# Performance work log

Measured on AMD Instinct MI355X. Metric: run time of the kernel, lower is better.

## Reference

```python
import jax, jax.numpy as jnp
import numpy as np

B, F = 4096, 16384          # batch, total features
G, S = 512, 32              # n_groups, group_size (F = G*S, contiguous partition)
UNITS = 1


def setup_inputs() -> dict:
    key = jax.random.key(0)
    k_x, k_w = jax.random.split(key)
    x = jax.random.normal(k_x, (B, F), dtype=jnp.float32)
    # contiguous non-overlapping groups: group g owns columns [g*S, (g+1)*S)
    group_idx = jnp.arange(G * S, dtype=jnp.int64).reshape(G, S)
    # per-group multiplicative-factor weights (GroupConnected.w, HeNormal ~ scaled normal)
    w_group = jax.random.normal(k_w, (G, S), dtype=jnp.float32) * jnp.sqrt(2.0 / S)
    # final Dense kernel, kernel_initializer=Ones in the original
    fc_kernel = jnp.ones((G, UNITS), dtype=jnp.float32)
    return {"x": x, "group_idx": group_idx, "w_group": w_group, "fc_kernel": fc_kernel}


def reference(x, group_idx, w_group, fc_kernel):
    # GroupConnected: per-group gather + weighted sum, vectorized as one gather + einsum.
    gathered = x[:, group_idx]                      # [B, G, S]
    gc = jnp.einsum('bgs,gs->bg', gathered, w_group)  # [B, G]
    # TibGroupLasso.fc: Dense(units, no bias)
    return gc @ fc_kernel                           # [B, units]
```

## Files before the change

kernel.cpp:

```cpp
#include <hip/hip_runtime.h>

#define BB 4096
#define FF 16384
#define GG 512
#define SS 32

typedef float v4f __attribute__((ext_vector_type(4)));

__global__ void build_v_kernel(const int* __restrict__ idx,
                               const float* __restrict__ w,
                               const float* __restrict__ fc,
                               float* __restrict__ v) {
    int i = blockIdx.x * blockDim.x + threadIdx.x;
    if (i < GG * SS) {
        v[idx[i]] = w[i] * fc[i >> 5];
    }
}

__global__ __launch_bounds__(256) void gemv_kernel(const float* __restrict__ x,
                                                   const float* __restrict__ v,
                                                   float* __restrict__ out) {
    const int wave = threadIdx.x >> 6;
    const int lane = threadIdx.x & 63;
    const int row  = (blockIdx.x << 2) + wave;

    const v4f* __restrict__ x4 = (const v4f*)(x + (size_t)row * FF);
    const v4f* __restrict__ v4 = (const v4f*)v;

    v4f acc0 = {0.0f, 0.0f, 0.0f, 0.0f};
    v4f acc1 = {0.0f, 0.0f, 0.0f, 0.0f};
    #pragma unroll 4
    for (int i = lane; i < FF / 4; i += 128) {
        v4f xa = __builtin_nontemporal_load(&x4[i]);
        v4f xb = __builtin_nontemporal_load(&x4[i + 64]);
        acc0 += xa * v4[i];
        acc1 += xb * v4[i + 64];
    }
    v4f acc = acc0 + acc1;
    float sum = (acc.x + acc.y) + (acc.z + acc.w);

    #pragma unroll
    for (int off = 32; off > 0; off >>= 1)
        sum += __shfl_down(sum, off, 64);

    if (lane == 0) out[row] = sum;
}

extern "C" void kernel_launch(void* const* d_in, const int* in_sizes, int n_in,
                              void* d_out, int out_size, void* d_ws, size_t ws_size,
                              hipStream_t stream) {
    const float* x   = (const float*)d_in[0];
    const int*   idx = (const int*)d_in[1];
    const float* w   = (const float*)d_in[2];
    const float* fc  = (const float*)d_in[3];
    float* out = (float*)d_out;
    float* v   = (float*)d_ws;

    build_v_kernel<<<(GG * SS + 255) / 256, 256, 0, stream>>>(idx, w, fc, v);
    gemv_kernel<<<BB / 4, 256, 0, stream>>>(x, v, out);
}
```

Measured before the change: 338.1 us.

## Split GEMV columns in halves, stage weight vector in LDS, add combine pass

Each block now handles four rows over one half of the feature dimension and first copies that half of the weight vector (32 KB) into shared memory. The kernel then reads the vector from LDS instead of global memory. Partial sums are written to workspace and a third kernel adds the two halves. This doubles the block count and cuts global traffic for the vector, at the cost of an extra launch, a per-block LDS fill with a barrier, and lower occupancy from the 32 KB of shared memory per block.

```diff
diff --git a/kernel.cpp b/kernel.cpp
--- a/kernel.cpp
+++ b/kernel.cpp
@@ -4,6 +4,7 @@
 #define FF 16384
 #define GG 512
 #define SS 32
+#define HALF (FF / 2)
 
 typedef float v4f __attribute__((ext_vector_type(4)));
 
@@ -17,24 +18,35 @@
     }
 }
 
-__global__ __launch_bounds__(256) void gemv_kernel(const float* __restrict__ x,
-                                                   const float* __restrict__ v,
-                                                   float* __restrict__ out) {
-    const int wave = threadIdx.x >> 6;
-    const int lane = threadIdx.x & 63;
-    const int row  = (blockIdx.x << 2) + wave;
+__global__ __launch_bounds__(256, 4) void gemv_kernel(const float* __restrict__ x,
+                                                      const float* __restrict__ v,
+                                                      float* __restrict__ part) {
+    __shared__ v4f vs[HALF / 4];
 
-    const v4f* __restrict__ x4 = (const v4f*)(x + (size_t)row * FF);
-    const v4f* __restrict__ v4 = (const v4f*)v;
+    const int c  = blockIdx.x & 1;
+    const int r0 = (blockIdx.x >> 1) << 2;
+    const int tid = threadIdx.x;
+
+    const v4f* __restrict__ vg = (const v4f*)(v + c * HALF);
+    #pragma unroll
+    for (int i = tid; i < HALF / 4; i += 256)
+        vs[i] = vg[i];
+    __syncthreads();
+
+    const int wave = tid >> 6;
+    const int lane = tid & 63;
+    const int row  = r0 + wave;
+
+    const v4f* __restrict__ x4 = (const v4f*)(x + (size_t)row * FF + c * HALF);
 
     v4f acc0 = {0.0f, 0.0f, 0.0f, 0.0f};
     v4f acc1 = {0.0f, 0.0f, 0.0f, 0.0f};
     #pragma unroll 4
-    for (int i = lane; i < FF / 4; i += 128) {
+    for (int i = lane; i < HALF / 4; i += 128) {
         v4f xa = __builtin_nontemporal_load(&x4[i]);
         v4f xb = __builtin_nontemporal_load(&x4[i + 64]);
-        acc0 += xa * v4[i];
-        acc1 += xb * v4[i + 64];
+        acc0 += xa * vs[i];
+        acc1 += xb * vs[i + 64];
     }
     v4f acc = acc0 + acc1;
     float sum = (acc.x + acc.y) + (acc.z + acc.w);
@@ -43,7 +55,13 @@
     for (int off = 32; off > 0; off >>= 1)
         sum += __shfl_down(sum, off, 64);
 
-    if (lane == 0) out[row] = sum;
+    if (lane == 0) part[c * BB + row] = sum;
+}
+
+__global__ void combine_kernel(const float* __restrict__ part,
+                               float* __restrict__ out) {
+    int i = blockIdx.x * blockDim.x + threadIdx.x;
+    if (i < BB) out[i] = part[i] + part[BB + i];
 }
 
 extern "C" void kernel_launch(void* const* d_in, const int* in_sizes, int n_in,
@@ -54,8 +72,10 @@
     const float* w   = (const float*)d_in[2];
     const float* fc  = (const float*)d_in[3];
     float* out = (float*)d_out;
-    float* v   = (float*)d_ws;
+    float* v    = (float*)d_ws;
+    float* part = v + FF;
 
     build_v_kernel<<<(GG * SS + 255) / 256, 256, 0, stream>>>(idx, w, fc, v);
-    gemv_kernel<<<BB / 4, 256, 0, stream>>>(x, v, out);
+    gemv_kernel<<<2 * (BB / 4), 256, 0, stream>>>(x, v, part);
+    combine_kernel<<<(BB + 255) / 256, 256, 0, stream>>>(part, out);
 }
```

New measurement: 337.0 us. No clear change (-0.3%).
